# Kernel tuning notes

Hardware: AMD Instinct MI355X
Metric: run time of the kernel (lower is better)

The kernel has to match this reference:

```python
import jax, jax.numpy as jnp
import numpy as np

GRID = 16            # spp grid (init kwarg)
K_MAX = 32           # max entries per cell (xy.shape[1] - 3)
B = 64               # number of graphs in batch
N_PER = 2048         # nodes per graph (equal-sized graphs)
D = 256              # input_dim
R = GRID * GRID      # max valid cell-rows per graph; valid rows come first


def setup_inputs() -> dict:
    key = jax.random.key(0)
    rng = np.random.default_rng(0)
    # xy layout per row: [grid_row, grid_col, count, idx_0 ... idx_{K_MAX-1}]
    # rows beyond the first R per graph are sentinel (-1) => original code breaks.
    xy = np.zeros((B, N_PER, 3 + K_MAX), dtype=np.int64)
    xy[:, :, 0] = -1
    cells = np.argsort(rng.random((B, R)), axis=1)  # unique cell per valid row
    xy[:, :R, 0] = cells // GRID
    xy[:, :R, 1] = cells % GRID
    xy[:, :R, 2] = rng.integers(1, K_MAX + 1, size=(B, R))
    xy[:, :R, 3:] = rng.integers(0, N_PER, size=(B, R, K_MAX))
    features = jax.random.normal(key, (B * N_PER, D), dtype=jnp.float32)
    nodes_per_graph = jnp.full((B,), N_PER, dtype=jnp.int64)
    return {"features": features,
            "xy": jnp.asarray(xy.reshape(B * N_PER, 3 + K_MAX)),
            "nodes_per_graph": nodes_per_graph}


def reference(features, xy, nodes_per_graph):
    Bn = nodes_per_graph.shape[0]
    n_per = features.shape[0] // Bn
    d = features.shape[1]
    F = features.reshape(Bn, n_per, d)                 # graph-local node feats
    xyb = xy.reshape(Bn, n_per, -1)[:, :R]             # valid rows are first R
    rows, cols, counts = xyb[..., 0], xyb[..., 1], xyb[..., 2]
    inds = xyb[..., 3:]                                # [B, R, K]
    valid = rows >= 0
    # per-cell gather of node features: [B, R, K, D]
    gathered = jax.vmap(lambda f, i: f[i])(F, inds)
    k_mask = (jnp.arange(inds.shape[-1])[None, None, :] < counts[..., None])
    denom = jnp.maximum(counts, 1).astype(features.dtype)[..., None]
    # mean readout over the first `count` entries
    pooled = (gathered * k_mask[..., None].astype(features.dtype)).sum(axis=2) / denom
    # scatter into dense grid; invalid rows routed to a dummy slot
    cell = jnp.where(valid, rows * GRID + cols, GRID * GRID)
    out = jnp.zeros((Bn, GRID * GRID + 1, d), features.dtype)
    out = out.at[jnp.arange(Bn)[:, None], cell].set(pooled)
    out = out[:, :GRID * GRID].reshape(Bn, GRID, GRID, d)
    return jnp.transpose(out, (0, 3, 1, 2))            # [B, D, GRID, GRID]
```

## Files before the change

kernel.cpp:

```cpp
#include <hip/hip_runtime.h>

#define GRIDN   16
#define KMAX    32
#define NPER    2048
#define DFEAT   256
#define RCELLS  256
#define XYS     35
#define CC      8

__device__ __forceinline__ void add4(float4& a, const float4& b) {
    a.x += b.x; a.y += b.y; a.z += b.z; a.w += b.w;
}

__global__ __launch_bounds__(256, 8) void spp_pool_kernel(
    const float* __restrict__ F,
    const int*   __restrict__ xy,
    float*       __restrict__ out)
{
    int blk    = blockIdx.x;
    int b      = blk >> 5;
    int c0     = (blk & 31) * CC;

    __shared__ float pooled[CC][DFEAT];
    __shared__ int   inds_l[CC][KMAX];
    __shared__ int   pos_l[CC];
    __shared__ int   cnt_l[CC];

    int tid = threadIdx.x;
    if (tid < CC) pos_l[tid] = -1;
    __syncthreads();

    {
        int r = tid;
        const int* xr = xy + ((size_t)b * NPER + (size_t)r) * XYS;
        int row = xr[0];
        if (row >= 0) {
            int cell = row * GRIDN + xr[1];
            if (cell >= c0 && cell < c0 + CC) {
                pos_l[cell - c0] = r;
                cnt_l[cell - c0] = xr[2];
            }
        }
    }
    __syncthreads();

    {
        int cl = tid >> 5;
        int k  = tid & 31;
        int r  = pos_l[cl];
        inds_l[cl][k] = (r >= 0) ? xy[((size_t)b * NPER + (size_t)r) * XYS + 3 + k] : 0;
    }
    __syncthreads();

    int wv   = tid >> 6;
    int lane = tid & 63;
    const float4* Fb4 = (const float4*)(F + ((size_t)b * NPER) * DFEAT);

    for (int j = 0; j < 2; ++j) {
        int cl = wv * 2 + j;
        int r  = pos_l[cl];
        float4 acc0 = make_float4(0.f, 0.f, 0.f, 0.f);
        float4 acc1 = make_float4(0.f, 0.f, 0.f, 0.f);
        float inv = 0.f;
        if (r >= 0) {
            int cnt = cnt_l[cl];
            const int* ip = inds_l[cl];
            int k = 0;
            for (; k + 8 <= cnt; k += 8) {
                int i0 = ip[k+0], i1 = ip[k+1], i2 = ip[k+2], i3 = ip[k+3];
                int i4 = ip[k+4], i5 = ip[k+5], i6 = ip[k+6], i7 = ip[k+7];
                float4 f0 = Fb4[(size_t)i0 * 64 + lane];
                float4 f1 = Fb4[(size_t)i1 * 64 + lane];
                float4 f2 = Fb4[(size_t)i2 * 64 + lane];
                float4 f3 = Fb4[(size_t)i3 * 64 + lane];
                float4 f4 = Fb4[(size_t)i4 * 64 + lane];
                float4 f5 = Fb4[(size_t)i5 * 64 + lane];
                float4 f6 = Fb4[(size_t)i6 * 64 + lane];
                float4 f7 = Fb4[(size_t)i7 * 64 + lane];
                add4(acc0, f0); add4(acc1, f1);
                add4(acc0, f2); add4(acc1, f3);
                add4(acc0, f4); add4(acc1, f5);
                add4(acc0, f6); add4(acc1, f7);
            }
            for (; k < cnt; ++k) {
                float4 f = Fb4[(size_t)ip[k] * 64 + lane];
                add4(acc0, f);
            }
            inv = 1.f / (float)(cnt > 0 ? cnt : 1);
        }
        float4 res;
        res.x = (acc0.x + acc1.x) * inv;
        res.y = (acc0.y + acc1.y) * inv;
        res.z = (acc0.z + acc1.z) * inv;
        res.w = (acc0.w + acc1.w) * inv;
        *(float4*)&pooled[cl][lane * 4] = res;
    }
    __syncthreads();

    {
        int d = tid;
        float* ob = out + (size_t)b * (DFEAT * RCELLS) + (size_t)d * RCELLS + c0;
        float4 v0, v1;
        v0.x = pooled[0][d]; v0.y = pooled[1][d];
        v0.z = pooled[2][d]; v0.w = pooled[3][d];
        v1.x = pooled[4][d]; v1.y = pooled[5][d];
        v1.z = pooled[6][d]; v1.w = pooled[7][d];
        *(float4*)(ob + 0) = v0;
        *(float4*)(ob + 4) = v1;
    }
}

extern "C" void kernel_launch(void* const* d_in, const int* in_sizes, int n_in,
                              void* d_out, int out_size, void* d_ws, size_t ws_size,
                              hipStream_t stream) {
    const float* F  = (const float*)d_in[0];
    const int*   xy = (const int*)d_in[1];
    float*       out = (float*)d_out;
    int B = in_sizes[2];
    dim3 grid(B * 32), block(256);
    hipLaunchKernelGGL(spp_pool_kernel, grid, block, 0, stream, F, xy, out);
}
```

Measured before the change: 222.9 us.

## Halve cells per block and remap blocks so each XCD handles contiguous graphs

Reduces cells per block from 8 to 4, doubling the grid so each wave gathers a single cell, which adds parallelism and memory-level concurrency. Block indices are remapped so that blocks on the same XCD (round-robin by blockIdx & 7) process contiguous graphs, aiming to keep each graph's feature rows in that XCD's L2. The tradeoff is that each block now scans the xy header rows for only 4 cells, so that redundant scan work doubles, and the output writes become narrower float4 stores.

```diff
diff --git a/kernel.cpp b/kernel.cpp
--- a/kernel.cpp
+++ b/kernel.cpp
@@ -6,7 +6,7 @@
 #define DFEAT   256
 #define RCELLS  256
 #define XYS     35
-#define CC      8
+#define CC      4
 
 __device__ __forceinline__ void add4(float4& a, const float4& b) {
     a.x += b.x; a.y += b.y; a.z += b.z; a.w += b.w;
@@ -15,11 +15,20 @@
 __global__ __launch_bounds__(256, 8) void spp_pool_kernel(
     const float* __restrict__ F,
     const int*   __restrict__ xy,
-    float*       __restrict__ out)
+    float*       __restrict__ out,
+    int B)
 {
-    int blk    = blockIdx.x;
-    int b      = blk >> 5;
-    int c0     = (blk & 31) * CC;
+    int bx  = blockIdx.x;
+    int b, c0;
+    if ((B & 7) == 0) {
+        int xcd = bx & 7;
+        int s   = bx >> 3;
+        b  = xcd * (B >> 3) + (s >> 6);
+        c0 = (s & 63) * CC;
+    } else {
+        b  = bx >> 6;
+        c0 = (bx & 63) * CC;
+    }
 
     __shared__ float pooled[CC][DFEAT];
     __shared__ int   inds_l[CC][KMAX];
@@ -35,16 +44,16 @@
         const int* xr = xy + ((size_t)b * NPER + (size_t)r) * XYS;
         int row = xr[0];
         if (row >= 0) {
-            int cell = row * GRIDN + xr[1];
-            if (cell >= c0 && cell < c0 + CC) {
-                pos_l[cell - c0] = r;
-                cnt_l[cell - c0] = xr[2];
+            int cl = row * GRIDN + xr[1] - c0;
+            if (cl >= 0 && cl < CC) {
+                pos_l[cl] = r;
+                cnt_l[cl] = xr[2];
             }
         }
     }
     __syncthreads();
 
-    {
+    if (tid < CC * KMAX) {
         int cl = tid >> 5;
         int k  = tid & 31;
         int r  = pos_l[cl];
@@ -54,13 +63,12 @@
 
     int wv   = tid >> 6;
     int lane = tid & 63;
-    const float4* Fb4 = (const float4*)(F + ((size_t)b * NPER) * DFEAT);
-
-    for (int j = 0; j < 2; ++j) {
-        int cl = wv * 2 + j;
+    const float4* Fb4 = (const float4*)(F + (size_t)b * NPER * DFEAT);
+    {
+        int cl = wv;
         int r  = pos_l[cl];
-        float4 acc0 = make_float4(0.f, 0.f, 0.f, 0.f);
-        float4 acc1 = make_float4(0.f, 0.f, 0.f, 0.f);
+        float4 a0 = make_float4(0.f,0.f,0.f,0.f);
+        float4 a1 = make_float4(0.f,0.f,0.f,0.f);
         float inv = 0.f;
         if (r >= 0) {
             int cnt = cnt_l[cl];
@@ -77,36 +85,31 @@
                 float4 f5 = Fb4[(size_t)i5 * 64 + lane];
                 float4 f6 = Fb4[(size_t)i6 * 64 + lane];
                 float4 f7 = Fb4[(size_t)i7 * 64 + lane];
-                add4(acc0, f0); add4(acc1, f1);
-                add4(acc0, f2); add4(acc1, f3);
-                add4(acc0, f4); add4(acc1, f5);
-                add4(acc0, f6); add4(acc1, f7);
+                add4(a0, f0); add4(a1, f1);
+                add4(a0, f2); add4(a1, f3);
+                add4(a0, f4); add4(a1, f5);
+                add4(a0, f6); add4(a1, f7);
             }
             for (; k < cnt; ++k) {
-                float4 f = Fb4[(size_t)ip[k] * 64 + lane];
-                add4(acc0, f);
+                add4(a0, Fb4[(size_t)ip[k] * 64 + lane]);
             }
             inv = 1.f / (float)(cnt > 0 ? cnt : 1);
         }
         float4 res;
-        res.x = (acc0.x + acc1.x) * inv;
-        res.y = (acc0.y + acc1.y) * inv;
-        res.z = (acc0.z + acc1.z) * inv;
-        res.w = (acc0.w + acc1.w) * inv;
+        res.x = (a0.x + a1.x) * inv;
+        res.y = (a0.y + a1.y) * inv;
+        res.z = (a0.z + a1.z) * inv;
+        res.w = (a0.w + a1.w) * inv;
         *(float4*)&pooled[cl][lane * 4] = res;
     }
     __syncthreads();
 
     {
         int d = tid;
-        float* ob = out + (size_t)b * (DFEAT * RCELLS) + (size_t)d * RCELLS + c0;
-        float4 v0, v1;
-        v0.x = pooled[0][d]; v0.y = pooled[1][d];
-        v0.z = pooled[2][d]; v0.w = pooled[3][d];
-        v1.x = pooled[4][d]; v1.y = pooled[5][d];
-        v1.z = pooled[6][d]; v1.w = pooled[7][d];
-        *(float4*)(ob + 0) = v0;
-        *(float4*)(ob + 4) = v1;
+        float4 v;
+        v.x = pooled[0][d]; v.y = pooled[1][d];
+        v.z = pooled[2][d]; v.w = pooled[3][d];
+        *(float4*)(out + (size_t)b * (DFEAT * RCELLS) + (size_t)d * RCELLS + c0) = v;
     }
 }
 
@@ -117,6 +120,6 @@
     const int*   xy = (const int*)d_in[1];
     float*       out = (float*)d_out;
     int B = in_sizes[2];
-    dim3 grid(B * 32), block(256);
-    hipLaunchKernelGGL(spp_pool_kernel, grid, block, 0, stream, F, xy, out);
+    dim3 grid(B * (RCELLS / CC)), block(256);
+    hipLaunchKernelGGL(spp_pool_kernel, grid, block, 0, stream, F, xy, out, B);
 }
```

Result: no change. 218.6 us (-1.9%).
